# Optimization experiments

Measured on AMD Instinct MI355X. Metric: run time of the kernel, lower is better.

## Reference

```python
import jax, jax.numpy as jnp
import numpy as np

N_NODES = 128   # num_nodes
BATCH = 4096
HIDDEN = 32     # fixed by the module's Linear(N+1, 32)


def setup_inputs() -> dict:
    key = jax.random.key(0)
    ks = jax.random.split(key, 8)
    N, B, H = N_NODES, BATCH, HIDDEN
    x = jax.random.normal(ks[0], (B, N), dtype=jnp.float32)
    # adjacency masks: A[b, :, j] = parent indicator of node j in sample b
    A = (jax.random.uniform(ks[1], (B, N, N)) < 0.3).astype(jnp.float32)
    # per-sample topological permutation
    order = jax.vmap(lambda k: jax.random.permutation(k, N))(
        jax.random.split(ks[2], B)).astype(jnp.int32)
    # intervention target per sample, -1 = no intervention
    do_idxs = jax.random.randint(ks[3], (B,), -1, N, dtype=jnp.int32)
    # externalized intervention noise (torch.normal in the original forward)
    u = jax.random.normal(ks[4], (B,), dtype=jnp.float32)
    # stacked per-node MLP params: Linear(N+1, 32) -> LeakyReLU -> Linear(32, 1)
    W1 = jax.random.normal(ks[5], (N, N + 1, H), dtype=jnp.float32) / np.sqrt(N + 1)
    b1 = jnp.zeros((N, H), dtype=jnp.float32)
    W2 = jax.random.normal(ks[6], (N, H, 1), dtype=jnp.float32) / np.sqrt(H)
    b2 = jnp.zeros((N, 1), dtype=jnp.float32)
    return dict(x=x, A=A, u=u, W1=W1, b1=b1, W2=W2, b2=b2,
                order=order, do_idxs=do_idxs)


def reference(x, A, u, W1, b1, W2, b2, order, do_idxs):
    B, N = x.shape
    bidx = jnp.arange(B)
    # set intervened entries: outputs[b, do_idxs[b]] = u[b] where do_idxs != -1
    outputs0 = jnp.where(do_idxs[:, None] == jnp.arange(N)[None, :],
                         u[:, None], jnp.zeros_like(x))

    def step(outputs, node):           # node: [B] current node per sample
        mask = A[bidx, :, node]        # [B, N] parent mask of this node
        ins = jnp.concatenate([mask * outputs,
                               x[bidx, node][:, None]], axis=1)  # [B, N+1]
        # per-node MLP gathered by node id (grouped tiny GEMMs)
        h = jax.nn.leaky_relu(jnp.einsum('bd,bdh->bh', ins, W1[node]) + b1[node])
        out = (jnp.einsum('bh,bho->bo', h, W2[node]) + b2[node])[:, 0]  # [B]
        # intervened samples keep their value u (they are skipped in the original)
        new_val = jnp.where(do_idxs == node, outputs[bidx, node], out)
        return outputs.at[bidx, node].set(new_val), None

    outputs, _ = jax.lax.scan(step, outputs0, order.T)  # sequential topo order
    return outputs
```

## Files before the change

kernel.cpp:

```cpp
#include <hip/hip_runtime.h>
#include <stdint.h>

#define NN 128
#define BB 4096
#define HH 32

typedef float f4 __attribute__((ext_vector_type(4)));

__global__ __launch_bounds__(256) void pack_bits(const float* __restrict__ A,
                                                 ulonglong2* __restrict__ bitsT) {
    const int tid = blockIdx.x * 256 + threadIdx.x;
    const int b   = tid >> 5;
    const int ng  = (tid & 31) << 2;
    const float* Ab = A + (size_t)b * (NN * NN) + ng;
    unsigned long long w0[4] = {0ull, 0ull, 0ull, 0ull};
    unsigned long long w1[4] = {0ull, 0ull, 0ull, 0ull};
#pragma unroll 8
    for (int d = 0; d < 64; ++d) {
        f4 v = __builtin_nontemporal_load((const f4*)(Ab + (size_t)d * NN));
        const unsigned long long bit = 1ull << d;
        if (v[0] != 0.f) w0[0] |= bit;
        if (v[1] != 0.f) w0[1] |= bit;
        if (v[2] != 0.f) w0[2] |= bit;
        if (v[3] != 0.f) w0[3] |= bit;
    }
#pragma unroll 8
    for (int d = 0; d < 64; ++d) {
        f4 v = __builtin_nontemporal_load((const f4*)(Ab + (size_t)(d + 64) * NN));
        const unsigned long long bit = 1ull << d;
        if (v[0] != 0.f) w1[0] |= bit;
        if (v[1] != 0.f) w1[1] |= bit;
        if (v[2] != 0.f) w1[2] |= bit;
        if (v[3] != 0.f) w1[3] |= bit;
    }
    ulonglong2* o = bitsT + b * NN + ng;
#pragma unroll
    for (int i = 0; i < 4; ++i) {
        ulonglong2 r; r.x = w0[i]; r.y = w1[i];
        o[i] = r;
    }
}

__global__ __launch_bounds__(64) void cond_mlp(
    const float* __restrict__ x, const float* __restrict__ u,
    const float* __restrict__ W1, const float* __restrict__ b1,
    const float* __restrict__ W2, const float* __restrict__ b2,
    const int* __restrict__ order, const int* __restrict__ do_idxs,
    const ulonglong2* __restrict__ bitsT, float* __restrict__ out)
{
    const int b = blockIdx.x;
    const int lane = threadIdx.x;
    const int j = lane & 31;
    const int half = lane >> 5;

    __shared__ float2 ent[132];

    const float ub = u[b];
    const int dob = do_idxs[b];
    float out0 = (dob == lane) ? ub : 0.f;
    float out1 = (dob == lane + 64) ? ub : 0.f;

    const int* ord = order + b * NN;
    const ulonglong2* bb = bitsT + (size_t)b * NN;

    const unsigned long long lanebit = 1ull << lane;
    const unsigned long long below = lanebit - 1ull;

    int node = ord[0];
    ulonglong2 bits = bb[node];

    for (int t = 0; t < NN; ++t) {
        const int node_n = (t < NN - 1) ? ord[t + 1] : 0;
        const ulonglong2 bits_n = bb[node_n];

        const float* Wn = W1 + (size_t)node * (NN + 1) * HH;
        const float w2v  = W2[node * HH + j];
        const float b1v  = b1[node * HH + j];
        const float xv   = x[b * NN + node];
        const float b2v  = b2[node];
        const float w1xv = Wn[NN * HH + j];

        unsigned long long bal0 = __ballot(out0 != 0.f) & bits.x;
        unsigned long long bal1 = __ballot(out1 != 0.f) & bits.y;
        const int c0 = __popcll(bal0);
        const int cnt = c0 + __popcll(bal1);
        if (bal0 & lanebit) {
            int p = __popcll(bal0 & below);
            ent[p] = make_float2(out0, __int_as_float(lane << 5));
        }
        if (bal1 & lanebit) {
            int p = c0 + __popcll(bal1 & below);
            ent[p] = make_float2(out1, __int_as_float((lane + 64) << 5));
        }
        const int cnt4 = (cnt + 3) & ~3;
        if (lane < cnt4 - cnt) ent[cnt + lane] = make_float2(0.f, __int_as_float(0));
        asm volatile("s_waitcnt lgkmcnt(0)" ::: "memory");

        float acc0 = 0.f, acc1 = 0.f;
        for (int k = 0; k < cnt4; k += 4) {
            float2 eA = ent[k + half];
            float2 eB = ent[k + 2 + half];
            acc0 += eA.x * Wn[__float_as_int(eA.y) + j];
            acc1 += eB.x * Wn[__float_as_int(eB.y) + j];
        }

        float acc = acc0 + acc1;
        acc += __shfl_xor(acc, 32);
        acc += xv * w1xv;
        acc += b1v;
        const float hv = (acc > 0.f) ? acc : 0.01f * acc;

        float p = hv * w2v;
        p += __int_as_float(__builtin_amdgcn_update_dpp(
                 0, __float_as_int(p), 0xB1, 0xF, 0xF, true));
        p += __int_as_float(__builtin_amdgcn_update_dpp(
                 0, __float_as_int(p), 0x4E, 0xF, 0xF, true));
        p += __int_as_float(__builtin_amdgcn_update_dpp(
                 0, __float_as_int(p), 0x141, 0xF, 0xF, true));
        p += __int_as_float(__builtin_amdgcn_update_dpp(
                 0, __float_as_int(p), 0x140, 0xF, 0xF, true));
        p += __shfl_xor(p, 16);
        const float outv = p + b2v;

        if (dob != node && lane == (node & 63)) {
            if (node < 64) out0 = outv; else out1 = outv;
        }
        node = node_n;
        bits = bits_n;
    }

    out[b * NN + lane] = out0;
    out[b * NN + 64 + lane] = out1;
}

extern "C" void kernel_launch(void* const* d_in, const int* in_sizes, int n_in,
                              void* d_out, int out_size, void* d_ws, size_t ws_size,
                              hipStream_t stream) {
    const float* x   = (const float*)d_in[0];
    const float* A   = (const float*)d_in[1];
    const float* u   = (const float*)d_in[2];
    const float* W1  = (const float*)d_in[3];
    const float* b1  = (const float*)d_in[4];
    const float* W2  = (const float*)d_in[5];
    const float* b2  = (const float*)d_in[6];
    const int* order = (const int*)d_in[7];
    const int* dox   = (const int*)d_in[8];

    ulonglong2* bitsT = (ulonglong2*)d_ws;

    pack_bits<<<(BB * 32) / 256, 256, 0, stream>>>(A, bitsT);
    cond_mlp<<<BB, 64, 0, stream>>>(x, u, W1, b1, W2, b2, order, dox,
                                    bitsT, (float*)d_out);
}
```

Baseline: 545.1 us.

## Replace LDS parent compaction with scalar bitmask walk and readlane gathers

Parent indices are no longer compacted into shared memory. Each step walks the wave-uniform ballot-and-mask bitmask with count-trailing-zeros and fetches each parent value straight from its owning lane with readlane. Weight loads are software-pipelined in groups of four. This removes the LDS writes, the wait and the cross-half shuffle reduction on the sequential critical path. In exchange, both wave halves now redundantly process every parent, so each lane does twice the multiply-adds and issues many more scalar instructions.

```diff
diff --git a/kernel.cpp b/kernel.cpp
--- a/kernel.cpp
+++ b/kernel.cpp
@@ -41,6 +41,25 @@
     }
 }
 
+#define PULL(dO, vO)                                                        \
+    {                                                                       \
+        const bool _s0 = (m0 != 0ull);                                      \
+        const unsigned long long _m = _s0 ? m0 : m1;                        \
+        const bool _ok = (_m != 0ull);                                      \
+        int _d = (int)__builtin_ctzll(_m | 0x8000000000000000ull);          \
+        _d = _ok ? _d : 0;                                                  \
+        const float _va = __int_as_float(__builtin_amdgcn_readlane(         \
+            __float_as_int(out0), _d));                                     \
+        const float _vb = __int_as_float(__builtin_amdgcn_readlane(         \
+            __float_as_int(out1), _d));                                     \
+        const float _v = _s0 ? _va : _vb;                                   \
+        vO = _ok ? _v : 0.f;                                                \
+        dO = _s0 ? _d : (_d + 64);                                          \
+        const unsigned long long _mn = _m & (_m - 1ull);                    \
+        m0 = _s0 ? _mn : m0;                                                \
+        m1 = _s0 ? m1 : _mn;                                                \
+    }
+
 __global__ __launch_bounds__(64) void cond_mlp(
     const float* __restrict__ x, const float* __restrict__ u,
     const float* __restrict__ W1, const float* __restrict__ b1,
@@ -51,9 +70,6 @@
     const int b = blockIdx.x;
     const int lane = threadIdx.x;
     const int j = lane & 31;
-    const int half = lane >> 5;
-
-    __shared__ float2 ent[132];
 
     const float ub = u[b];
     const int dob = do_idxs[b];
@@ -62,9 +78,6 @@
 
     const int* ord = order + b * NN;
     const ulonglong2* bb = bitsT + (size_t)b * NN;
-
-    const unsigned long long lanebit = 1ull << lane;
-    const unsigned long long below = lanebit - 1ull;
 
     int node = ord[0];
     ulonglong2 bits = bb[node];
@@ -80,32 +93,52 @@
         const float b2v  = b2[node];
         const float w1xv = Wn[NN * HH + j];
 
-        unsigned long long bal0 = __ballot(out0 != 0.f) & bits.x;
-        unsigned long long bal1 = __ballot(out1 != 0.f) & bits.y;
-        const int c0 = __popcll(bal0);
-        const int cnt = c0 + __popcll(bal1);
-        if (bal0 & lanebit) {
-            int p = __popcll(bal0 & below);
-            ent[p] = make_float2(out0, __int_as_float(lane << 5));
-        }
-        if (bal1 & lanebit) {
-            int p = c0 + __popcll(bal1 & below);
-            ent[p] = make_float2(out1, __int_as_float((lane + 64) << 5));
-        }
-        const int cnt4 = (cnt + 3) & ~3;
-        if (lane < cnt4 - cnt) ent[cnt + lane] = make_float2(0.f, __int_as_float(0));
-        asm volatile("s_waitcnt lgkmcnt(0)" ::: "memory");
+        const unsigned int bxl = __builtin_amdgcn_readfirstlane((unsigned int)bits.x);
+        const unsigned int bxh = __builtin_amdgcn_readfirstlane((unsigned int)(bits.x >> 32));
+        const unsigned int byl = __builtin_amdgcn_readfirstlane((unsigned int)bits.y);
+        const unsigned int byh = __builtin_amdgcn_readfirstlane((unsigned int)(bits.y >> 32));
+        unsigned long long m0 = __ballot(out0 != 0.f) &
+                                (((unsigned long long)bxh << 32) | bxl);
+        unsigned long long m1 = __ballot(out1 != 0.f) &
+                                (((unsigned long long)byh << 32) | byl);
+        const int cnt = __popcll(m0) + __popcll(m1);
 
-        float acc0 = 0.f, acc1 = 0.f;
-        for (int k = 0; k < cnt4; k += 4) {
-            float2 eA = ent[k + half];
-            float2 eB = ent[k + 2 + half];
-            acc0 += eA.x * Wn[__float_as_int(eA.y) + j];
-            acc1 += eB.x * Wn[__float_as_int(eB.y) + j];
+        float acc = 0.f;
+        const int G = (cnt + 3) >> 2;
+        if (G) {
+            int dA0, dA1, dA2, dA3, dB0, dB1, dB2, dB3;
+            float vA0, vA1, vA2, vA3, vB0, vB1, vB2, vB3;
+            float wA0, wA1, wA2, wA3, wB0, wB1, wB2, wB3;
+
+            PULL(dA0, vA0) PULL(dA1, vA1) PULL(dA2, vA2) PULL(dA3, vA3)
+            wA0 = Wn[(dA0 << 5) + j];
+            wA1 = Wn[(dA1 << 5) + j];
+            wA2 = Wn[(dA2 << 5) + j];
+            wA3 = Wn[(dA3 << 5) + j];
+
+            for (int g = 1; g < G; g += 2) {
+                PULL(dB0, vB0) PULL(dB1, vB1) PULL(dB2, vB2) PULL(dB3, vB3)
+                wB0 = Wn[(dB0 << 5) + j];
+                wB1 = Wn[(dB1 << 5) + j];
+                wB2 = Wn[(dB2 << 5) + j];
+                wB3 = Wn[(dB3 << 5) + j];
+
+                acc += vA0 * wA0; acc += vA1 * wA1;
+                acc += vA2 * wA2; acc += vA3 * wA3;
+
+                PULL(dA0, vA0) PULL(dA1, vA1) PULL(dA2, vA2) PULL(dA3, vA3)
+                wA0 = Wn[(dA0 << 5) + j];
+                wA1 = Wn[(dA1 << 5) + j];
+                wA2 = Wn[(dA2 << 5) + j];
+                wA3 = Wn[(dA3 << 5) + j];
+
+                acc += vB0 * wB0; acc += vB1 * wB1;
+                acc += vB2 * wB2; acc += vB3 * wB3;
+            }
+            acc += vA0 * wA0; acc += vA1 * wA1;
+            acc += vA2 * wA2; acc += vA3 * wA3;
         }
 
-        float acc = acc0 + acc1;
-        acc += __shfl_xor(acc, 32);
         acc += xv * w1xv;
         acc += b1v;
         const float hv = (acc > 0.f) ? acc : 0.01f * acc;
```

Measured after the change: 1.058 ms. 1.94x slower.

## Track nonzero parents in scalar mask, defer last output, unroll gather loop

Applied to the files above, without the earlier changes.

Replaces the per-step ballot over output values with a scalar bitmask of written nodes, using mbcnt for compaction. It defers the previous step's output write and adds its contribution separately, so the dependency on the last result is taken off the critical path into LDS. The variable-length gather loop becomes fixed 32-entry unrolled blocks padded with zeros, which issues loads in batches. It also sets launch bounds occupancy to 4 and moves uniform values to scalar registers. The cost is extra zero-padded work when there are few parents, plus more register use.

```diff
diff --git a/kernel.cpp b/kernel.cpp
--- a/kernel.cpp
+++ b/kernel.cpp
@@ -41,7 +41,12 @@
     }
 }
 
-__global__ __launch_bounds__(64) void cond_mlp(
+__device__ __forceinline__ int mbcnt64(unsigned long long m) {
+    return __builtin_amdgcn_mbcnt_hi((unsigned int)(m >> 32),
+           __builtin_amdgcn_mbcnt_lo((unsigned int)m, 0));
+}
+
+__global__ __launch_bounds__(64, 4) void cond_mlp(
     const float* __restrict__ x, const float* __restrict__ u,
     const float* __restrict__ W1, const float* __restrict__ b1,
     const float* __restrict__ W2, const float* __restrict__ b2,
@@ -56,21 +61,30 @@
     __shared__ float2 ent[132];
 
     const float ub = u[b];
-    const int dob = do_idxs[b];
+    const int dob = __builtin_amdgcn_readfirstlane(do_idxs[b]);
     float out0 = (dob == lane) ? ub : 0.f;
     float out1 = (dob == lane + 64) ? ub : 0.f;
 
+    unsigned long long nz0 = (dob >= 0 && dob < 64) ? (1ull << dob) : 0ull;
+    unsigned long long nz1 = (dob >= 64) ? (1ull << (dob - 64)) : 0ull;
+
     const int* ord = order + b * NN;
     const ulonglong2* bb = bitsT + (size_t)b * NN;
 
     const unsigned long long lanebit = 1ull << lane;
-    const unsigned long long below = lanebit - 1ull;
-
-    int node = ord[0];
+    const float fidx0 = __int_as_float(lane << 5);
+    const float fidx1 = __int_as_float((lane + 64) << 5);
+
+    int node = __builtin_amdgcn_readfirstlane(ord[0]);
     ulonglong2 bits = bb[node];
 
+    int node_prev = 0;
+    float outv_prev = 0.f;
+
     for (int t = 0; t < NN; ++t) {
-        const int node_n = (t < NN - 1) ? ord[t + 1] : 0;
+        const bool have_prev = (t > 0);
+        const int node_n = (t < NN - 1)
+            ? __builtin_amdgcn_readfirstlane(ord[t + 1]) : 0;
         const ulonglong2 bits_n = bb[node_n];
 
         const float* Wn = W1 + (size_t)node * (NN + 1) * HH;
@@ -79,36 +93,90 @@
         const float xv   = x[b * NN + node];
         const float b2v  = b2[node];
         const float w1xv = Wn[NN * HH + j];
-
-        unsigned long long bal0 = __ballot(out0 != 0.f) & bits.x;
-        unsigned long long bal1 = __ballot(out1 != 0.f) & bits.y;
-        const int c0 = __popcll(bal0);
-        const int cnt = c0 + __popcll(bal1);
-        if (bal0 & lanebit) {
-            int p = __popcll(bal0 & below);
-            ent[p] = make_float2(out0, __int_as_float(lane << 5));
-        }
-        if (bal1 & lanebit) {
-            int p = c0 + __popcll(bal1 & below);
-            ent[p] = make_float2(out1, __int_as_float((lane + 64) << 5));
-        }
+        const int   frow = (have_prev ? node_prev : 0) << 5;
+        const float wfr  = Wn[frow + j];
+
+        const unsigned int bxl = __builtin_amdgcn_readfirstlane((unsigned int)bits.x);
+        const unsigned int bxh = __builtin_amdgcn_readfirstlane((unsigned int)(bits.x >> 32));
+        const unsigned int byl = __builtin_amdgcn_readfirstlane((unsigned int)bits.y);
+        const unsigned int byh = __builtin_amdgcn_readfirstlane((unsigned int)(bits.y >> 32));
+        const unsigned long long bw0 = ((unsigned long long)bxh << 32) | bxl;
+        const unsigned long long bw1 = ((unsigned long long)byh << 32) | byl;
+        const unsigned long long m0 = nz0 & bw0;
+        const unsigned long long m1 = nz1 & bw1;
+        const int c0 = __popcll(m0);
+        const int cnt = c0 + __popcll(m1);
         const int cnt4 = (cnt + 3) & ~3;
-        if (lane < cnt4 - cnt) ent[cnt + lane] = make_float2(0.f, __int_as_float(0));
+
+        const int p0 = mbcnt64(m0);
+        if (m0 & lanebit) ent[p0] = make_float2(out0, fidx0);
+        const int p1 = c0 + mbcnt64(m1);
+        if (m1 & lanebit) ent[p1] = make_float2(out1, fidx1);
+        const int top = (cnt4 <= 32) ? 32 : ((cnt4 <= 64) ? 64 : cnt4);
+        const int pp = cnt + lane;
+        if (pp < top) ent[pp] = make_float2(0.f, __int_as_float(0));
+
+        if (have_prev && dob != node_prev && lane == (node_prev & 63)) {
+            if (node_prev < 64) out0 = outv_prev; else out1 = outv_prev;
+        }
+        if (have_prev) {
+            if (node_prev < 64) nz0 |= 1ull << node_prev;
+            else                nz1 |= 1ull << (node_prev - 64);
+        }
+
         asm volatile("s_waitcnt lgkmcnt(0)" ::: "memory");
 
-        float acc0 = 0.f, acc1 = 0.f;
-        for (int k = 0; k < cnt4; k += 4) {
-            float2 eA = ent[k + half];
-            float2 eB = ent[k + 2 + half];
-            acc0 += eA.x * Wn[__float_as_int(eA.y) + j];
-            acc1 += eB.x * Wn[__float_as_int(eB.y) + j];
-        }
-
-        float acc = acc0 + acc1;
-        acc += __shfl_xor(acc, 32);
-        acc += xv * w1xv;
-        acc += b1v;
-        const float hv = (acc > 0.f) ? acc : 0.01f * acc;
+        float acc;
+        {
+            float2 e[16];
+#pragma unroll
+            for (int i = 0; i < 16; ++i) e[i] = ent[2 * i + half];
+            float w[16];
+#pragma unroll
+            for (int i = 0; i < 16; ++i) w[i] = Wn[__float_as_int(e[i].y) + j];
+            float a0 = 0.f, a1 = 0.f, a2 = 0.f, a3 = 0.f;
+#pragma unroll
+            for (int i = 0; i < 16; i += 4) {
+                a0 += e[i].x     * w[i];
+                a1 += e[i + 1].x * w[i + 1];
+                a2 += e[i + 2].x * w[i + 2];
+                a3 += e[i + 3].x * w[i + 3];
+            }
+            acc = (a0 + a1) + (a2 + a3);
+        }
+        if (cnt4 > 32) {
+            float2 e[16];
+#pragma unroll
+            for (int i = 0; i < 16; ++i) e[i] = ent[32 + 2 * i + half];
+            float w[16];
+#pragma unroll
+            for (int i = 0; i < 16; ++i) w[i] = Wn[__float_as_int(e[i].y) + j];
+            float a0 = 0.f, a1 = 0.f, a2 = 0.f, a3 = 0.f;
+#pragma unroll
+            for (int i = 0; i < 16; i += 4) {
+                a0 += e[i].x     * w[i];
+                a1 += e[i + 1].x * w[i + 1];
+                a2 += e[i + 2].x * w[i + 2];
+                a3 += e[i + 3].x * w[i + 3];
+            }
+            acc += (a0 + a1) + (a2 + a3);
+        }
+        if (cnt4 > 64) {
+            for (int k = 64; k < cnt4; k += 4) {
+                float2 eA = ent[k + half];
+                float2 eB = ent[k + 2 + half];
+                acc += eA.x * Wn[__float_as_int(eA.y) + j];
+                acc += eB.x * Wn[__float_as_int(eB.y) + j];
+            }
+        }
+
+        float accT = acc + __shfl_xor(acc, 32);
+        const bool fc = have_prev && (dob != node_prev) &&
+            (((node_prev < 64) ? (bw0 >> node_prev) : (bw1 >> (node_prev - 64))) & 1ull);
+        accT += (fc ? outv_prev : 0.f) * wfr;
+        accT += xv * w1xv;
+        accT += b1v;
+        const float hv = (accT > 0.f) ? accT : 0.01f * accT;
 
         float p = hv * w2v;
         p += __int_as_float(__builtin_amdgcn_update_dpp(
@@ -122,11 +190,14 @@
         p += __shfl_xor(p, 16);
         const float outv = p + b2v;
 
-        if (dob != node && lane == (node & 63)) {
-            if (node < 64) out0 = outv; else out1 = outv;
-        }
+        outv_prev = outv;
+        node_prev = node;
         node = node_n;
         bits = bits_n;
+    }
+
+    if (dob != node_prev && lane == (node_prev & 63)) {
+        if (node_prev < 64) out0 = outv_prev; else out1 = outv_prev;
     }
 
     out[b * NN + lane] = out0;
```

Result: no change. 544.2 us (-0.2%).

## Software-pipeline sequential node steps with double-buffered parent lists and deferred output

Applied to the files above, without the earlier changes.

Restructures the per-sample sequential loop so the parent-entry list for step t+1 is built, and its weight gathers issued, while step t is still reducing. It double-buffers the shared entry list, keeps the first 32 entries in registers, and tracks nonzero outputs with scalar bitmasks instead of ballots. The just-computed node value is applied as a separate rank-1 correction term, so the next list can be built before that value exists. The goal is to hide global-load latency on the serial dependency chain, at the cost of more registers, a fixed 32-entry gather that may load unused padding, and more complex bookkeeping.

```diff
diff --git a/kernel.cpp b/kernel.cpp
--- a/kernel.cpp
+++ b/kernel.cpp
@@ -41,7 +41,114 @@
     }
 }
 
-__global__ __launch_bounds__(64) void cond_mlp(
+__device__ __forceinline__ int mbcnt64(unsigned long long m) {
+    return __builtin_amdgcn_mbcnt_hi((unsigned int)(m >> 32),
+           __builtin_amdgcn_mbcnt_lo((unsigned int)m, 0));
+}
+__device__ __forceinline__ unsigned long long rfl64(unsigned long long v) {
+    unsigned int lo = __builtin_amdgcn_readfirstlane((unsigned int)v);
+    unsigned int hi = __builtin_amdgcn_readfirstlane((unsigned int)(v >> 32));
+    return ((unsigned long long)hi << 32) | lo;
+}
+
+#define STEP(T, ECUR, ENXT, BCUR, BNXT)                                      \
+  {                                                                          \
+    const float* Wn_cur = W1 + (size_t)node0 * ((NN + 1) * HH);              \
+                   \
+    float wv[16];                                                            \
+    _Pragma("unroll")                                                        \
+    for (int i = 0; i < 16; ++i)                                             \
+        wv[i] = Wn_cur[__float_as_int(ECUR[i].y) + j];                       \
+                                  \
+    if ((T) > 0) {                                                           \
+        if (dob != pend_node && lane == (pend_node & 63)) {                  \
+            if (pend_node < 64) out0 = pend_val; else out1 = pend_val;       \
+        }                                                                    \
+        if (pend_node < 64) nz0 |= 1ull << pend_node;                        \
+        else                nz1 |= 1ull << (pend_node - 64);                 \
+    }                                                                        \
+               \
+    const unsigned long long bw0n = rfl64(vbn.x);                            \
+    const unsigned long long bw1n = rfl64(vbn.y);                            \
+    const unsigned long long m0 = nz0 & bw0n;                                \
+    const unsigned long long m1 = nz1 & bw1n;                                \
+    const int c0n  = __popcll(m0);                                           \
+    const int cntn = c0n + __popcll(m1);                                     \
+    const int cnt4n = (cntn + 3) & ~3;                                       \
+                      \
+    {                                                                        \
+        const int p0 = mbcnt64(m0);                                          \
+        if (m0 & lanebit) entb[BNXT][p0] = make_float2(out0, fidx0);         \
+        const int p1 = c0n + mbcnt64(m1);                                    \
+        if (m1 & lanebit) entb[BNXT][p1] = make_float2(out1, fidx1);         \
+        const int top = (cnt4n <= 32) ? 32 : cnt4n;                          \
+        const int pp = cntn + lane;                                          \
+        if (pp < top) entb[BNXT][pp] = make_float2(0.f, __int_as_float(0));  \
+    }                                                                        \
+    asm volatile("s_waitcnt lgkmcnt(0)" ::: "memory");                       \
+                         \
+    _Pragma("unroll")                                                        \
+    for (int i = 0; i < 16; ++i) ENXT[i] = entb[BNXT][2 * i + half];         \
+           \
+    const int node2 = ((T) + 2 < NN)                                         \
+        ? __builtin_amdgcn_readfirstlane(ord[(T) + 2]) : 0;                  \
+    const ulonglong2 vb2 = bb[node2];                                        \
+    const float* Wn_nxt = W1 + (size_t)node1 * ((NN + 1) * HH);              \
+    const float w2v_n  = W2[node1 * HH + j];                                 \
+    const float b1v_n  = b1[node1 * HH + j];                                 \
+    const float xv_n   = x[b * NN + node1];                                  \
+    const float b2v_n  = b2[node1];                                          \
+    const float w1xv_n = Wn_nxt[NN * HH + j];                                \
+    const float wfr_n  = Wn_nxt[(node0 << 5) + j];                           \
+                     \
+    float a0 = 0.f, a1 = 0.f, a2 = 0.f, a3 = 0.f;                            \
+    _Pragma("unroll")                                                        \
+    for (int i = 0; i < 16; i += 4) {                                        \
+        a0 += ECUR[i].x     * wv[i];                                         \
+        a1 += ECUR[i + 1].x * wv[i + 1];                                     \
+        a2 += ECUR[i + 2].x * wv[i + 2];                                     \
+        a3 += ECUR[i + 3].x * wv[i + 3];                                     \
+    }                                                                        \
+    float acc = (a0 + a1) + (a2 + a3);                                       \
+          \
+    if (cnt4_c > 32) {                                                       \
+        for (int k = 32; k < cnt4_c; k += 4) {                               \
+            float2 ea = entb[BCUR][k + half];                                \
+            float2 eb = entb[BCUR][k + 2 + half];                            \
+            acc += ea.x * Wn_cur[__float_as_int(ea.y) + j];                  \
+            acc += eb.x * Wn_cur[__float_as_int(eb.y) + j];                  \
+        }                                                                    \
+    }                                                                        \
+                                                       \
+    float accT = acc + __shfl_xor(acc, 32);                                  \
+    const bool fc = ((T) > 0) && (dob != pend_node) &&                       \
+        ((((pend_node < 64) ? (bw0c >> pend_node)                            \
+                            : (bw1c >> (pend_node - 64)))) & 1ull);          \
+    accT += (fc ? pend_val : 0.f) * wfr;                                     \
+    accT += xv * w1xv;                                                       \
+    accT += b1v;                                                             \
+    const float hv = (accT > 0.f) ? accT : 0.01f * accT;                     \
+    float pr = hv * w2v;                                                     \
+    pr += __int_as_float(__builtin_amdgcn_update_dpp(                        \
+             0, __float_as_int(pr), 0xB1, 0xF, 0xF, true));                  \
+    pr += __int_as_float(__builtin_amdgcn_update_dpp(                        \
+             0, __float_as_int(pr), 0x4E, 0xF, 0xF, true));                  \
+    pr += __int_as_float(__builtin_amdgcn_update_dpp(                        \
+             0, __float_as_int(pr), 0x141, 0xF, 0xF, true));                 \
+    pr += __int_as_float(__builtin_amdgcn_update_dpp(                        \
+             0, __float_as_int(pr), 0x140, 0xF, 0xF, true));                 \
+    pr += __shfl_xor(pr, 16);                                                \
+    const float outv = pr + b2v;                                             \
+    pend_node = node0; pend_val = outv;                                      \
+                                                              \
+    node0 = node1; node1 = node2;                                            \
+    bw0c = bw0n; bw1c = bw1n; vbn = vb2;                                     \
+    w2v = w2v_n; b1v = b1v_n; xv = xv_n; b2v = b2v_n;                        \
+    w1xv = w1xv_n; wfr = wfr_n;                                              \
+    cnt4_c = cnt4n;                                                          \
+  }
+
+__global__ __launch_bounds__(64, 4) void cond_mlp(
     const float* __restrict__ x, const float* __restrict__ u,
     const float* __restrict__ W1, const float* __restrict__ b1,
     const float* __restrict__ W2, const float* __restrict__ b2,
@@ -53,80 +160,68 @@
     const int j = lane & 31;
     const int half = lane >> 5;
 
-    __shared__ float2 ent[132];
+    __shared__ float2 entb[2][132];
 
     const float ub = u[b];
-    const int dob = do_idxs[b];
+    const int dob = __builtin_amdgcn_readfirstlane(do_idxs[b]);
     float out0 = (dob == lane) ? ub : 0.f;
     float out1 = (dob == lane + 64) ? ub : 0.f;
 
+    unsigned long long nz0 = (dob >= 0 && dob < 64) ? (1ull << dob) : 0ull;
+    unsigned long long nz1 = (dob >= 64) ? (1ull << (dob - 64)) : 0ull;
+
     const int* ord = order + b * NN;
     const ulonglong2* bb = bitsT + (size_t)b * NN;
 
     const unsigned long long lanebit = 1ull << lane;
-    const unsigned long long below = lanebit - 1ull;
-
-    int node = ord[0];
-    ulonglong2 bits = bb[node];
-
-    for (int t = 0; t < NN; ++t) {
-        const int node_n = (t < NN - 1) ? ord[t + 1] : 0;
-        const ulonglong2 bits_n = bb[node_n];
-
-        const float* Wn = W1 + (size_t)node * (NN + 1) * HH;
-        const float w2v  = W2[node * HH + j];
-        const float b1v  = b1[node * HH + j];
-        const float xv   = x[b * NN + node];
-        const float b2v  = b2[node];
-        const float w1xv = Wn[NN * HH + j];
-
-        unsigned long long bal0 = __ballot(out0 != 0.f) & bits.x;
-        unsigned long long bal1 = __ballot(out1 != 0.f) & bits.y;
-        const int c0 = __popcll(bal0);
-        const int cnt = c0 + __popcll(bal1);
-        if (bal0 & lanebit) {
-            int p = __popcll(bal0 & below);
-            ent[p] = make_float2(out0, __int_as_float(lane << 5));
-        }
-        if (bal1 & lanebit) {
-            int p = c0 + __popcll(bal1 & below);
-            ent[p] = make_float2(out1, __int_as_float((lane + 64) << 5));
-        }
-        const int cnt4 = (cnt + 3) & ~3;
-        if (lane < cnt4 - cnt) ent[cnt + lane] = make_float2(0.f, __int_as_float(0));
-        asm volatile("s_waitcnt lgkmcnt(0)" ::: "memory");
-
-        float acc0 = 0.f, acc1 = 0.f;
-        for (int k = 0; k < cnt4; k += 4) {
-            float2 eA = ent[k + half];
-            float2 eB = ent[k + 2 + half];
-            acc0 += eA.x * Wn[__float_as_int(eA.y) + j];
-            acc1 += eB.x * Wn[__float_as_int(eB.y) + j];
-        }
-
-        float acc = acc0 + acc1;
-        acc += __shfl_xor(acc, 32);
-        acc += xv * w1xv;
-        acc += b1v;
-        const float hv = (acc > 0.f) ? acc : 0.01f * acc;
-
-        float p = hv * w2v;
-        p += __int_as_float(__builtin_amdgcn_update_dpp(
-                 0, __float_as_int(p), 0xB1, 0xF, 0xF, true));
-        p += __int_as_float(__builtin_amdgcn_update_dpp(
-                 0, __float_as_int(p), 0x4E, 0xF, 0xF, true));
-        p += __int_as_float(__builtin_amdgcn_update_dpp(
-                 0, __float_as_int(p), 0x141, 0xF, 0xF, true));
-        p += __int_as_float(__builtin_amdgcn_update_dpp(
-                 0, __float_as_int(p), 0x140, 0xF, 0xF, true));
-        p += __shfl_xor(p, 16);
-        const float outv = p + b2v;
-
-        if (dob != node && lane == (node & 63)) {
-            if (node < 64) out0 = outv; else out1 = outv;
-        }
-        node = node_n;
-        bits = bits_n;
+    const float fidx0 = __int_as_float(lane << 5);
+    const float fidx1 = __int_as_float((lane + 64) << 5);
+
+    int node0 = __builtin_amdgcn_readfirstlane(ord[0]);
+    int node1 = __builtin_amdgcn_readfirstlane(ord[1]);
+    const ulonglong2 vb0 = bb[node0];
+    ulonglong2 vbn = bb[node1];
+
+    unsigned long long bw0c = rfl64(vb0.x);
+    unsigned long long bw1c = rfl64(vb0.y);
+    int cnt4_c;
+    {
+        const unsigned long long m0 = nz0 & bw0c;
+        const unsigned long long m1 = nz1 & bw1c;
+        const int c0 = __popcll(m0);
+        const int cnt = c0 + __popcll(m1);
+        cnt4_c = (cnt + 3) & ~3;
+        const int p0 = mbcnt64(m0);
+        if (m0 & lanebit) entb[0][p0] = make_float2(out0, fidx0);
+        const int p1 = c0 + mbcnt64(m1);
+        if (m1 & lanebit) entb[0][p1] = make_float2(out1, fidx1);
+        const int top = (cnt4_c <= 32) ? 32 : cnt4_c;
+        const int pp = cnt + lane;
+        if (pp < top) entb[0][pp] = make_float2(0.f, __int_as_float(0));
+    }
+    asm volatile("s_waitcnt lgkmcnt(0)" ::: "memory");
+    float2 eA[16], eB[16];
+#pragma unroll
+    for (int i = 0; i < 16; ++i) eA[i] = entb[0][2 * i + half];
+
+    const float* Wn0 = W1 + (size_t)node0 * ((NN + 1) * HH);
+    float w2v  = W2[node0 * HH + j];
+    float b1v  = b1[node0 * HH + j];
+    float xv   = x[b * NN + node0];
+    float b2v  = b2[node0];
+    float w1xv = Wn0[NN * HH + j];
+    float wfr  = 0.f;
+
+    int pend_node = 0;
+    float pend_val = 0.f;
+
+    for (int t = 0; t < NN; t += 2) {
+        STEP(t,     eA, eB, 0, 1)
+        STEP(t + 1, eB, eA, 1, 0)
+    }
+
+    if (dob != pend_node && lane == (pend_node & 63)) {
+        if (pend_node < 64) out0 = pend_val; else out1 = pend_val;
     }
 
     out[b * NN + lane] = out0;
```

Measured after the change: 528.6 us. -3.0%, faster.
